# Performance work log

Hardware: AMD Instinct MI355X
Metric: run time of the kernel (lower is better)

## Reference

```python
import jax, jax.numpy as jnp
import numpy as np

N_USERS = 100000
N_ITEMS = 50000
N_EDGES = 2000000
D = 64
EPS = 1e-12  # F.normalize default eps


def setup_inputs() -> dict:
    key = jax.random.key(0)
    k1, k2, k3, k4 = jax.random.split(key, 4)
    x = jax.random.normal(k1, (N_USERS + N_ITEMS, D), dtype=jnp.float32)
    beta = jax.random.normal(k2, (N_USERS,), dtype=jnp.float32) * 0.1
    u = jax.random.randint(k3, (N_EDGES,), 0, N_USERS)
    i = jax.random.randint(k4, (N_EDGES,), 0, N_ITEMS)
    ones = jnp.ones((N_EDGES,), jnp.float32)
    # degree vectors (clamped to >=1 so sqrt-normalization is well-defined)
    du = jnp.maximum(jax.ops.segment_sum(ones, u, num_segments=N_USERS), 1.0)
    di = jnp.maximum(jax.ops.segment_sum(ones, i, num_segments=N_ITEMS), 1.0)
    return {"x": x, "beta": beta, "du": du, "di": di, "u": u, "i": i}


def reference(x, beta, du, di, u, i):
    # split into user/item blocks
    xu, xi = x[:N_USERS], x[N_USERS:]
    # row-wise L2 normalize (torch F.normalize)
    z = x / jnp.maximum(jnp.linalg.norm(x, axis=1, keepdims=True), EPS)
    zu, zi = z[:N_USERS], z[N_USERS:]
    # per-edge score and omega weight: 4/((1+e^-s)(1+e^s)) == 4*sig(s)*(1-sig(s))
    s = jnp.sum(zu[u] * zi[i], axis=1) - beta[u]          # [E]
    sig = jax.nn.sigmoid(s)
    w = 4.0 * sig * (1.0 - sig)
    w = w / jnp.sqrt(du[u]) / jnp.sqrt(di[i])             # degree normalization
    w = w[:, None]                                        # [E,1]
    # scatter-add aggregation back to users and items
    dxu = jax.ops.segment_sum(w * xi[i], u, num_segments=N_USERS)  # [n,D]
    dxi = jax.ops.segment_sum(w * xu[u], i, num_segments=N_ITEMS)  # [m,D]
    return jnp.concatenate([dxu, dxi], axis=0)
```

## Files before the change

kernel.cpp:

```cpp
#include <hip/hip_runtime.h>
#include <math.h>

#define N_USERS 100000
#define N_ITEMS 50000
#define NR      150000
#define N_EDGES 2000000
#define D       64
#define EPS     1e-12f

#define UPAD 64
#define IPAD 80
#define OVF_CAP 4096

#define NPART 8
#define UPP 12500
#define IPP 6250
#define FILL_BPP 256

#define SCAL_OFF 0u
#define XH_OFF   2400000u
#define CNT_OFF  21600000u
#define UBKT_OFF 22200000u
#define IBKT_OFF 35000000u
#define OVFC_OFF 51000000u
#define OVF_OFF  51000004u
#define WS_A3    51016388u

#define C_SCAL 0u
#define C_HEAD 2400000u
#define C_NXTU 3000000u
#define C_NXTI 11000000u
#define WS_C   19000000u

__device__ __forceinline__ unsigned short f2bf(float v) {
    unsigned int b = __float_as_uint(v);
    b += 0x7FFFu + ((b >> 16) & 1u);
    return (unsigned short)(b >> 16);
}
#define BF_LO(w) __uint_as_float((w) << 16)
#define BF_HI(w) __uint_as_float((w) & 0xFFFF0000u)

__global__ void prep_kernel(const float* __restrict__ x,
                            const float* __restrict__ beta,
                            const float* __restrict__ du,
                            const float* __restrict__ di,
                            float4* __restrict__ scal,
                            unsigned short* __restrict__ xh) {
    int gid  = blockIdx.x * blockDim.x + threadIdx.x;
    int r    = gid >> 6;
    int lane = gid & 63;
    if (r >= NR) return;

    float v = x[r * D + lane];
    xh[r * D + lane] = f2bf(v);

    float ss = v * v;
    #pragma unroll
    for (int m = 32; m >= 1; m >>= 1) ss += __shfl_xor(ss, m);

    if (lane == 0) {
        float invn = 1.0f / fmaxf(sqrtf(ss), EPS);
        float deg  = (r < N_USERS) ? du[r] : di[r - N_USERS];
        float b    = (r < N_USERS) ? beta[r] : 0.0f;
        scal[r] = make_float4(invn, rsqrtf(deg), b, 0.0f);
    }
}

__global__ void fillx_kernel(const int* __restrict__ u,
                             const int* __restrict__ i,
                             int* __restrict__ cnt,
                             unsigned short* __restrict__ ubkt,
                             unsigned int* __restrict__ ibkt,
                             int* __restrict__ ovfc,
                             int* __restrict__ ovf) {
    int p   = blockIdx.x & (NPART - 1);
    int q   = blockIdx.x >> 3;
    int tid = q * blockDim.x + threadIdx.x;
    const int stride = FILL_BPP * 256;

    int ulo = p * UPP, uhi = ulo + UPP;
    int ilo = p * IPP, ihi = ilo + IPP;

    for (int e = tid; e < N_EDGES; e += stride) {
        int uu = __builtin_nontemporal_load(u + e);
        int ii = __builtin_nontemporal_load(i + e);

        if (uu >= ulo && uu < uhi) {
            int s = atomicAdd(&cnt[uu], 1);
            if (s < UPAD) {
                ubkt[(size_t)uu * UPAD + s] = (unsigned short)ii;
            } else {
                int pp = atomicAdd(ovfc, 1);
                if (pp < OVF_CAP) ovf[pp] = (e << 1);
            }
        }
        if (ii >= ilo && ii < ihi) {
            int s = atomicAdd(&cnt[N_USERS + ii], 1);
            if (s < IPAD) {
                ibkt[(size_t)ii * IPAD + s] = (unsigned int)uu;
            } else {
                int pp = atomicAdd(ovfc, 1);
                if (pp < OVF_CAP) ovf[pp] = (e << 1) | 1;
            }
        }
    }
}

__global__ void gatherU_kernel(const unsigned short* __restrict__ xh,
                               const float4* __restrict__ scal,
                               const int* __restrict__ cnt,
                               const unsigned short* __restrict__ ubkt,
                               float* __restrict__ out) {
    int gid  = blockIdx.x * blockDim.x + threadIdx.x;
    int r    = gid >> 6;
    int lane = gid & 63;
    if (r >= N_USERS) return;

    int g = lane >> 3;
    int q = lane & 7;

    float4 sc = scal[r];
    uint4 hs = *(const uint4*)(xh + (size_t)r * D + q * 8);
    float xs0 = BF_LO(hs.x), xs1 = BF_HI(hs.x);
    float xs2 = BF_LO(hs.y), xs3 = BF_HI(hs.y);
    float xs4 = BF_LO(hs.z), xs5 = BF_HI(hs.z);
    float xs6 = BF_LO(hs.w), xs7 = BF_HI(hs.w);

    int deg = cnt[r];
    if (deg > UPAD) deg = UPAD;
    int iters = (deg + 7) >> 3;

    float a0=0.f,a1=0.f,a2=0.f,a3=0.f,a4=0.f,a5=0.f,a6=0.f,a7=0.f;

    for (int it = 0; it < iters; ++it) {
        int idx = it * 8 + g;
        bool valid = (idx < deg);
        int nb = N_USERS + (int)ubkt[(size_t)r * UPAD + (valid ? idx : 0)];

        float4 so = scal[nb];
        uint4 ho = *(const uint4*)(xh + (size_t)nb * D + q * 8);
        float o0 = BF_LO(ho.x), o1 = BF_HI(ho.x);
        float o2 = BF_LO(ho.y), o3 = BF_HI(ho.y);
        float o4 = BF_LO(ho.z), o5 = BF_HI(ho.z);
        float o6 = BF_LO(ho.w), o7 = BF_HI(ho.w);

        float p = xs0*o0 + xs1*o1 + xs2*o2 + xs3*o3
                + xs4*o4 + xs5*o5 + xs6*o6 + xs7*o7;
        p += __shfl_xor(p, 1);
        p += __shfl_xor(p, 2);
        p += __shfl_xor(p, 4);

        float sv  = p * sc.x * so.x - sc.z;
        float sig = 1.0f / (1.0f + __expf(-sv));
        float w   = 4.0f * sig * (1.0f - sig) * sc.y * so.y;
        w = valid ? w : 0.0f;

        a0 = fmaf(w, o0, a0); a1 = fmaf(w, o1, a1);
        a2 = fmaf(w, o2, a2); a3 = fmaf(w, o3, a3);
        a4 = fmaf(w, o4, a4); a5 = fmaf(w, o5, a5);
        a6 = fmaf(w, o6, a6); a7 = fmaf(w, o7, a7);
    }

    #pragma unroll
    for (int m = 8; m <= 32; m <<= 1) {
        a0 += __shfl_xor(a0, m); a1 += __shfl_xor(a1, m);
        a2 += __shfl_xor(a2, m); a3 += __shfl_xor(a3, m);
        a4 += __shfl_xor(a4, m); a5 += __shfl_xor(a5, m);
        a6 += __shfl_xor(a6, m); a7 += __shfl_xor(a7, m);
    }

    if (g == 0) {
        float4* o4p = (float4*)(out + (size_t)r * D + q * 8);
        o4p[0] = make_float4(a0, a1, a2, a3);
        o4p[1] = make_float4(a4, a5, a6, a7);
    }
}

__global__ void gatherI_kernel(const unsigned short* __restrict__ xh,
                               const float4* __restrict__ scal,
                               const int* __restrict__ cnt,
                               const unsigned int* __restrict__ ibkt,
                               float* __restrict__ out) {
    int gid  = blockIdx.x * blockDim.x + threadIdx.x;
    int ri   = gid >> 6;
    int lane = gid & 63;
    if (ri >= N_ITEMS) return;
    int r = N_USERS + ri;

    int g = lane >> 3;
    int q = lane & 7;

    float4 sc = scal[r];
    uint4 hs = *(const uint4*)(xh + (size_t)r * D + q * 8);
    float xs0 = BF_LO(hs.x), xs1 = BF_HI(hs.x);
    float xs2 = BF_LO(hs.y), xs3 = BF_HI(hs.y);
    float xs4 = BF_LO(hs.z), xs5 = BF_HI(hs.z);
    float xs6 = BF_LO(hs.w), xs7 = BF_HI(hs.w);

    int deg = cnt[r];
    if (deg > IPAD) deg = IPAD;
    int iters = (deg + 7) >> 3;

    float a0=0.f,a1=0.f,a2=0.f,a3=0.f,a4=0.f,a5=0.f,a6=0.f,a7=0.f;

    for (int it = 0; it < iters; ++it) {
        int idx = it * 8 + g;
        bool valid = (idx < deg);
        int nb = (int)ibkt[(size_t)ri * IPAD + (valid ? idx : 0)];

        float4 so = scal[nb];
        uint4 ho = *(const uint4*)(xh + (size_t)nb * D + q * 8);
        float o0 = BF_LO(ho.x), o1 = BF_HI(ho.x);
        float o2 = BF_LO(ho.y), o3 = BF_HI(ho.y);
        float o4 = BF_LO(ho.z), o5 = BF_HI(ho.z);
        float o6 = BF_LO(ho.w), o7 = BF_HI(ho.w);

        float p = xs0*o0 + xs1*o1 + xs2*o2 + xs3*o3
                + xs4*o4 + xs5*o5 + xs6*o6 + xs7*o7;
        p += __shfl_xor(p, 1);
        p += __shfl_xor(p, 2);
        p += __shfl_xor(p, 4);

        float sv  = p * sc.x * so.x - so.z;
        float sig = 1.0f / (1.0f + __expf(-sv));
        float w   = 4.0f * sig * (1.0f - sig) * sc.y * so.y;
        w = valid ? w : 0.0f;

        a0 = fmaf(w, o0, a0); a1 = fmaf(w, o1, a1);
        a2 = fmaf(w, o2, a2); a3 = fmaf(w, o3, a3);
        a4 = fmaf(w, o4, a4); a5 = fmaf(w, o5, a5);
        a6 = fmaf(w, o6, a6); a7 = fmaf(w, o7, a7);
    }

    #pragma unroll
    for (int m = 8; m <= 32; m <<= 1) {
        a0 += __shfl_xor(a0, m); a1 += __shfl_xor(a1, m);
        a2 += __shfl_xor(a2, m); a3 += __shfl_xor(a3, m);
        a4 += __shfl_xor(a4, m); a5 += __shfl_xor(a5, m);
        a6 += __shfl_xor(a6, m); a7 += __shfl_xor(a7, m);
    }

    if (g == 0) {
        float4* o4p = (float4*)(out + (size_t)r * D + q * 8);
        o4p[0] = make_float4(a0, a1, a2, a3);
        o4p[1] = make_float4(a4, a5, a6, a7);
    }
}

__global__ void ovf_kernel(const float* __restrict__ x,
                           const float4* __restrict__ scal,
                           const int* __restrict__ u,
                           const int* __restrict__ i,
                           const int* __restrict__ ovfc,
                           const int* __restrict__ ovf,
                           float* __restrict__ out) {
    int n = *ovfc;
    if (n > OVF_CAP) n = OVF_CAP;
    int gid  = blockIdx.x * blockDim.x + threadIdx.x;
    int wave = gid >> 6;
    int lane = gid & 63;
    int nw   = (gridDim.x * blockDim.x) >> 6;

    for (int k = wave; k < n; k += nw) {
        int pk = ovf[k];
        int e = pk >> 1, side = pk & 1;
        int uu = u[e];
        int ir = N_USERS + i[e];
        float xu = x[uu * D + lane];
        float xi = x[ir * D + lane];
        float p = xu * xi;
        #pragma unroll
        for (int m = 32; m >= 1; m >>= 1) p += __shfl_xor(p, m);
        float4 su = scal[uu];
        float4 si = scal[ir];
        float sv  = p * su.x * si.x - su.z;
        float sig = 1.0f / (1.0f + __expf(-sv));
        float w   = 4.0f * sig * (1.0f - sig) * su.y * si.y;
        if (side == 0) atomicAdd(&out[(size_t)uu * D + lane], w * xi);
        else           atomicAdd(&out[(size_t)ir * D + lane], w * xu);
    }
}

__global__ void scal_kernel(const float* __restrict__ x,
                            const float* __restrict__ beta,
                            const float* __restrict__ du,
                            const float* __restrict__ di,
                            float4* __restrict__ scal) {
    int gid  = blockIdx.x * blockDim.x + threadIdx.x;
    int r    = gid >> 6;
    int lane = gid & 63;
    if (r >= NR) return;
    float v  = x[r * D + lane];
    float ss = v * v;
    #pragma unroll
    for (int m = 32; m >= 1; m >>= 1) ss += __shfl_xor(ss, m);
    if (lane == 0) {
        float invn = 1.0f / fmaxf(sqrtf(ss), EPS);
        float deg  = (r < N_USERS) ? du[r] : di[r - N_USERS];
        float b    = (r < N_USERS) ? beta[r] : 0.0f;
        scal[r] = make_float4(invn, rsqrtf(deg), b, 0.0f);
    }
}

__global__ void link_kernel(const int* __restrict__ u,
                            const int* __restrict__ i,
                            int* __restrict__ head,
                            int* __restrict__ next_u,
                            int* __restrict__ next_i) {
    int e = blockIdx.x * blockDim.x + threadIdx.x;
    if (e >= N_EDGES) return;
    int uu = u[e];
    int ii = N_USERS + i[e];
    next_u[e] = atomicExch(&head[uu], e);
    next_i[e] = atomicExch(&head[ii], e);
}

__global__ void gather_kernel(const float4* __restrict__ x4,
                              const float4* __restrict__ scal,
                              const int* __restrict__ head,
                              const int* __restrict__ next_u,
                              const int* __restrict__ next_i,
                              const int* __restrict__ u,
                              const int* __restrict__ i,
                              float4* __restrict__ out4) {
    int gid  = blockIdx.x * blockDim.x + threadIdx.x;
    int r    = gid >> 6;
    int lane = gid & 63;
    if (r >= NR) return;
    int g = lane >> 4;
    int q = lane & 15;
    bool isu = (r < N_USERS);
    const int* __restrict__ nxt = isu ? next_u : next_i;
    const int* __restrict__ oid = isu ? i : u;
    int obase = isu ? N_USERS : 0;
    float4 sc = scal[r];
    float4 xs = x4[r * 16 + q];
    float4 acc = make_float4(0.f, 0.f, 0.f, 0.f);
    int e  = head[r];
    int c0 = e; { int t = nxt[(c0 >= 0) ? c0 : 0]; e = (c0 >= 0) ? t : -1; }
    int c1 = e; { int t = nxt[(c1 >= 0) ? c1 : 0]; e = (c1 >= 0) ? t : -1; }
    int c2 = e; { int t = nxt[(c2 >= 0) ? c2 : 0]; e = (c2 >= 0) ? t : -1; }
    int c3 = e; { int t = nxt[(c3 >= 0) ? c3 : 0]; e = (c3 >= 0) ? t : -1; }
    while (c0 >= 0) {
        int n0 = e; { int t = nxt[(n0 >= 0) ? n0 : 0]; e = (n0 >= 0) ? t : -1; }
        int n1 = e; { int t = nxt[(n1 >= 0) ? n1 : 0]; e = (n1 >= 0) ? t : -1; }
        int n2 = e; { int t = nxt[(n2 >= 0) ? n2 : 0]; e = (n2 >= 0) ? t : -1; }
        int n3 = e; { int t = nxt[(n3 >= 0) ? n3 : 0]; e = (n3 >= 0) ? t : -1; }
        int eg = (g == 0) ? c0 : (g == 1) ? c1 : (g == 2) ? c2 : c3;
        bool valid = (eg >= 0);
        int  es = valid ? eg : c0;
        int  nb = obase + oid[es];
        float4 so = scal[nb];
        float4 xo = x4[nb * 16 + q];
        float p = xs.x * xo.x + xs.y * xo.y + xs.z * xo.z + xs.w * xo.w;
        p += __shfl_xor(p, 1);
        p += __shfl_xor(p, 2);
        p += __shfl_xor(p, 4);
        p += __shfl_xor(p, 8);
        float b   = isu ? sc.z : so.z;
        float sv  = p * sc.x * so.x - b;
        float sig = 1.0f / (1.0f + __expf(-sv));
        float w   = 4.0f * sig * (1.0f - sig) * sc.y * so.y;
        w = valid ? w : 0.0f;
        acc.x = fmaf(w, xo.x, acc.x);
        acc.y = fmaf(w, xo.y, acc.y);
        acc.z = fmaf(w, xo.z, acc.z);
        acc.w = fmaf(w, xo.w, acc.w);
        c0 = n0; c1 = n1; c2 = n2; c3 = n3;
    }
    acc.x += __shfl_xor(acc.x, 16); acc.y += __shfl_xor(acc.y, 16);
    acc.z += __shfl_xor(acc.z, 16); acc.w += __shfl_xor(acc.w, 16);
    acc.x += __shfl_xor(acc.x, 32); acc.y += __shfl_xor(acc.y, 32);
    acc.z += __shfl_xor(acc.z, 32); acc.w += __shfl_xor(acc.w, 32);
    if (g == 0) out4[r * 16 + q] = acc;
}

__global__ void norm_kernel(const float* __restrict__ x,
                            float* __restrict__ invn,
                            int nrows) {
    int gid  = blockIdx.x * blockDim.x + threadIdx.x;
    int wave = gid >> 6;
    int lane = gid & 63;
    if (wave >= nrows) return;
    float v  = x[wave * D + lane];
    float ss = v * v;
    #pragma unroll
    for (int m = 32; m >= 1; m >>= 1) ss += __shfl_xor(ss, m);
    if (lane == 0) invn[wave] = 1.0f / fmaxf(sqrtf(ss), EPS);
}

__global__ void edge_kernel(const float* __restrict__ x,
                            const float* __restrict__ beta,
                            const float* __restrict__ du,
                            const float* __restrict__ di,
                            const int*   __restrict__ u,
                            const int*   __restrict__ i,
                            const float* __restrict__ invn,
                            float* __restrict__ out) {
    int gid  = blockIdx.x * blockDim.x + threadIdx.x;
    int wave = gid >> 6;
    int lane = gid & 63;
    if (wave >= N_EDGES) return;
    int uu = u[wave];
    int ii = i[wave];
    const float xu = x[uu * D + lane];
    const float xi = x[(N_USERS + ii) * D + lane];
    float p = xu * xi;
    #pragma unroll
    for (int m = 32; m >= 1; m >>= 1) p += __shfl_xor(p, m);
    float s   = p * invn[uu] * invn[N_USERS + ii] - beta[uu];
    float sig = 1.0f / (1.0f + __expf(-s));
    float w   = 4.0f * sig * (1.0f - sig) * rsqrtf(du[uu]) * rsqrtf(di[ii]);
    atomicAdd(&out[uu * D + lane],             w * xi);
    atomicAdd(&out[(N_USERS + ii) * D + lane], w * xu);
}

extern "C" void kernel_launch(void* const* d_in, const int* in_sizes, int n_in,
                              void* d_out, int out_size, void* d_ws, size_t ws_size,
                              hipStream_t stream) {
    const float* x    = (const float*)d_in[0];
    const float* beta = (const float*)d_in[1];
    const float* du   = (const float*)d_in[2];
    const float* di   = (const float*)d_in[3];
    const int*   u    = (const int*)d_in[4];
    const int*   i    = (const int*)d_in[5];
    float* out = (float*)d_out;
    char*  ws  = (char*)d_ws;

    if (ws_size >= (size_t)WS_A3) {
        float4*         scal = (float4*)(ws + SCAL_OFF);
        unsigned short* xh   = (unsigned short*)(ws + XH_OFF);
        int*            cnt  = (int*)(ws + CNT_OFF);
        unsigned short* ubkt = (unsigned short*)(ws + UBKT_OFF);
        unsigned int*   ibkt = (unsigned int*)(ws + IBKT_OFF);
        int*            ovfc = (int*)(ws + OVFC_OFF);
        int*            ovf  = (int*)(ws + OVF_OFF);

        prep_kernel<<<(NR + 3) / 4, 256, 0, stream>>>(x, beta, du, di, scal, xh);
        hipMemsetAsync(cnt, 0, (size_t)NR * sizeof(int), stream);
        hipMemsetAsync(ovfc, 0, sizeof(int), stream);
        fillx_kernel<<<NPART * FILL_BPP, 256, 0, stream>>>(u, i, cnt, ubkt, ibkt, ovfc, ovf);
        gatherU_kernel<<<(N_USERS + 3) / 4, 256, 0, stream>>>(xh, scal, cnt, ubkt, out);
        gatherI_kernel<<<(N_ITEMS + 3) / 4, 256, 0, stream>>>(xh, scal, cnt, ibkt, out);
        ovf_kernel<<<64, 256, 0, stream>>>(x, scal, u, i, ovfc, ovf, out);
    } else if (ws_size >= (size_t)WS_C) {
        float4* scal   = (float4*)(ws + C_SCAL);
        int*    head   = (int*)(ws + C_HEAD);
        int*    next_u = (int*)(ws + C_NXTU);
        int*    next_i = (int*)(ws + C_NXTI);

        scal_kernel<<<(NR + 3) / 4, 256, 0, stream>>>(x, beta, du, di, scal);
        hipMemsetAsync(head, 0xFF, (size_t)NR * sizeof(int), stream);
        link_kernel<<<(N_EDGES + 255) / 256, 256, 0, stream>>>(u, i, head, next_u, next_i);
        gather_kernel<<<(NR + 3) / 4, 256, 0, stream>>>((const float4*)x, scal, head,
                                                        next_u, next_i, u, i, (float4*)out);
    } else {
        float* invn = (float*)ws;
        hipMemsetAsync(d_out, 0, (size_t)out_size * sizeof(float), stream);
        norm_kernel<<<(NR + 3) / 4, 256, 0, stream>>>(x, invn, NR);
        edge_kernel<<<(N_EDGES + 3) / 4, 256, 0, stream>>>(x, beta, du, di, u, i, invn, out);
    }
}
```

Before: 317.6 us.

## Fuse prep into fill kernel, merge user/item gathers, halve fill partitions

Merges the prep pass into the bucket-fill kernel as extra blocks, so row normalization and bf16 conversion run alongside the edge bucketing. The separate user and item gather kernels become one launch. Each fill block now scans the edge list twice over two smaller node sub-ranges, aiming at better cache locality for the atomics and bucket writes at the cost of reading the edge arrays twice. The item bucket pad drops from 80 to 64, shrinking the workspace but sending more edges to the overflow atomic path, which is capped at 4096 entries.

```diff
diff --git a/kernel.cpp b/kernel.cpp
--- a/kernel.cpp
+++ b/kernel.cpp
@@ -9,22 +9,26 @@
 #define EPS     1e-12f
 
 #define UPAD 64
-#define IPAD 80
+#define IPAD 64
 #define OVF_CAP 4096
 
 #define NPART 8
-#define UPP 12500
-#define IPP 6250
+#define NSUB  2
+#define NCHUNK (NPART * NSUB)
+#define UCH (N_USERS / NCHUNK)
+#define ICH (N_ITEMS / NCHUNK)
 #define FILL_BPP 256
+#define FILL_BLOCKS (NPART * FILL_BPP)
+#define PREP_BLOCKS ((NR + 3) / 4)
 
 #define SCAL_OFF 0u
 #define XH_OFF   2400000u
 #define CNT_OFF  21600000u
 #define UBKT_OFF 22200000u
 #define IBKT_OFF 35000000u
-#define OVFC_OFF 51000000u
-#define OVF_OFF  51000004u
-#define WS_A3    51016388u
+#define OVFC_OFF 47800000u
+#define OVF_OFF  47800004u
+#define WS_A4    47816388u
 
 #define C_SCAL 0u
 #define C_HEAD 2400000u
@@ -40,81 +44,88 @@
 #define BF_LO(w) __uint_as_float((w) << 16)
 #define BF_HI(w) __uint_as_float((w) & 0xFFFF0000u)
 
-__global__ void prep_kernel(const float* __restrict__ x,
-                            const float* __restrict__ beta,
-                            const float* __restrict__ du,
-                            const float* __restrict__ di,
-                            float4* __restrict__ scal,
-                            unsigned short* __restrict__ xh) {
-    int gid  = blockIdx.x * blockDim.x + threadIdx.x;
-    int r    = gid >> 6;
-    int lane = gid & 63;
-    if (r >= NR) return;
-
-    float v = x[r * D + lane];
-    xh[r * D + lane] = f2bf(v);
-
-    float ss = v * v;
-    #pragma unroll
-    for (int m = 32; m >= 1; m >>= 1) ss += __shfl_xor(ss, m);
-
-    if (lane == 0) {
-        float invn = 1.0f / fmaxf(sqrtf(ss), EPS);
-        float deg  = (r < N_USERS) ? du[r] : di[r - N_USERS];
-        float b    = (r < N_USERS) ? beta[r] : 0.0f;
-        scal[r] = make_float4(invn, rsqrtf(deg), b, 0.0f);
-    }
-}
-
-__global__ void fillx_kernel(const int* __restrict__ u,
-                             const int* __restrict__ i,
-                             int* __restrict__ cnt,
-                             unsigned short* __restrict__ ubkt,
-                             unsigned int* __restrict__ ibkt,
-                             int* __restrict__ ovfc,
-                             int* __restrict__ ovf) {
-    int p   = blockIdx.x & (NPART - 1);
-    int q   = blockIdx.x >> 3;
-    int tid = q * blockDim.x + threadIdx.x;
-    const int stride = FILL_BPP * 256;
-
-    int ulo = p * UPP, uhi = ulo + UPP;
-    int ilo = p * IPP, ihi = ilo + IPP;
-
-    for (int e = tid; e < N_EDGES; e += stride) {
-        int uu = __builtin_nontemporal_load(u + e);
-        int ii = __builtin_nontemporal_load(i + e);
-
-        if (uu >= ulo && uu < uhi) {
-            int s = atomicAdd(&cnt[uu], 1);
-            if (s < UPAD) {
-                ubkt[(size_t)uu * UPAD + s] = (unsigned short)ii;
-            } else {
-                int pp = atomicAdd(ovfc, 1);
-                if (pp < OVF_CAP) ovf[pp] = (e << 1);
+__global__ void fillprep_kernel(const float* __restrict__ x,
+                                const float* __restrict__ beta,
+                                const float* __restrict__ du,
+                                const float* __restrict__ di,
+                                float4* __restrict__ scal,
+                                unsigned short* __restrict__ xh,
+                                const int* __restrict__ u,
+                                const int* __restrict__ i,
+                                int* __restrict__ cnt,
+                                unsigned short* __restrict__ ubkt,
+                                unsigned int* __restrict__ ibkt,
+                                int* __restrict__ ovfc,
+                                int* __restrict__ ovf) {
+    if (blockIdx.x < FILL_BLOCKS) {
+        int p   = blockIdx.x & (NPART - 1);
+        int qb  = blockIdx.x >> 3;
+        int tid = qb * blockDim.x + threadIdx.x;
+        const int stride = FILL_BPP * 256;
+
+        #pragma unroll
+        for (int sub = 0; sub < NSUB; ++sub) {
+            int c   = p * NSUB + sub;
+            int ulo = c * UCH, uhi = ulo + UCH;
+            int ilo = c * ICH, ihi = ilo + ICH;
+
+            for (int e = tid; e < N_EDGES; e += stride) {
+                int uu = __builtin_nontemporal_load(u + e);
+                int ii = __builtin_nontemporal_load(i + e);
+
+                if (uu >= ulo && uu < uhi) {
+                    int s = atomicAdd(&cnt[uu], 1);
+                    if (s < UPAD) {
+                        ubkt[(size_t)uu * UPAD + s] = (unsigned short)ii;
+                    } else {
+                        int pp = atomicAdd(ovfc, 1);
+                        if (pp < OVF_CAP) ovf[pp] = (e << 1);
+                    }
+                }
+                if (ii >= ilo && ii < ihi) {
+                    int s = atomicAdd(&cnt[N_USERS + ii], 1);
+                    if (s < IPAD) {
+                        ibkt[(size_t)ii * IPAD + s] = (unsigned int)uu;
+                    } else {
+                        int pp = atomicAdd(ovfc, 1);
+                        if (pp < OVF_CAP) ovf[pp] = (e << 1) | 1;
+                    }
+                }
             }
         }
-        if (ii >= ilo && ii < ihi) {
-            int s = atomicAdd(&cnt[N_USERS + ii], 1);
-            if (s < IPAD) {
-                ibkt[(size_t)ii * IPAD + s] = (unsigned int)uu;
-            } else {
-                int pp = atomicAdd(ovfc, 1);
-                if (pp < OVF_CAP) ovf[pp] = (e << 1) | 1;
-            }
+    } else {
+        int b    = blockIdx.x - FILL_BLOCKS;
+        int gid  = b * blockDim.x + threadIdx.x;
+        int r    = gid >> 6;
+        int lane = gid & 63;
+        if (r >= NR) return;
+
+        float v = x[r * D + lane];
+        xh[r * D + lane] = f2bf(v);
+
+        float ss = v * v;
+        #pragma unroll
+        for (int m = 32; m >= 1; m >>= 1) ss += __shfl_xor(ss, m);
+
+        if (lane == 0) {
+            float invn = 1.0f / fmaxf(sqrtf(ss), EPS);
+            float deg  = (r < N_USERS) ? du[r] : di[r - N_USERS];
+            float bb   = (r < N_USERS) ? beta[r] : 0.0f;
+            scal[r] = make_float4(invn, rsqrtf(deg), bb, 0.0f);
         }
     }
 }
 
-__global__ void gatherU_kernel(const unsigned short* __restrict__ xh,
+__global__ void gatherA_kernel(const unsigned short* __restrict__ xh,
                                const float4* __restrict__ scal,
                                const int* __restrict__ cnt,
                                const unsigned short* __restrict__ ubkt,
+                               const unsigned int* __restrict__ ibkt,
                                float* __restrict__ out) {
     int gid  = blockIdx.x * blockDim.x + threadIdx.x;
     int r    = gid >> 6;
     int lane = gid & 63;
-    if (r >= N_USERS) return;
+    if (r >= NR) return;
 
     int g = lane >> 3;
     int q = lane & 7;
@@ -126,110 +137,75 @@
     float xs4 = BF_LO(hs.z), xs5 = BF_HI(hs.z);
     float xs6 = BF_LO(hs.w), xs7 = BF_HI(hs.w);
 
-    int deg = cnt[r];
-    if (deg > UPAD) deg = UPAD;
-    int iters = (deg + 7) >> 3;
-
     float a0=0.f,a1=0.f,a2=0.f,a3=0.f,a4=0.f,a5=0.f,a6=0.f,a7=0.f;
 
-    for (int it = 0; it < iters; ++it) {
-        int idx = it * 8 + g;
-        bool valid = (idx < deg);
-        int nb = N_USERS + (int)ubkt[(size_t)r * UPAD + (valid ? idx : 0)];
-
-        float4 so = scal[nb];
-        uint4 ho = *(const uint4*)(xh + (size_t)nb * D + q * 8);
-        float o0 = BF_LO(ho.x), o1 = BF_HI(ho.x);
-        float o2 = BF_LO(ho.y), o3 = BF_HI(ho.y);
-        float o4 = BF_LO(ho.z), o5 = BF_HI(ho.z);
-        float o6 = BF_LO(ho.w), o7 = BF_HI(ho.w);
-
-        float p = xs0*o0 + xs1*o1 + xs2*o2 + xs3*o3
-                + xs4*o4 + xs5*o5 + xs6*o6 + xs7*o7;
-        p += __shfl_xor(p, 1);
-        p += __shfl_xor(p, 2);
-        p += __shfl_xor(p, 4);
-
-        float sv  = p * sc.x * so.x - sc.z;
-        float sig = 1.0f / (1.0f + __expf(-sv));
-        float w   = 4.0f * sig * (1.0f - sig) * sc.y * so.y;
-        w = valid ? w : 0.0f;
-
-        a0 = fmaf(w, o0, a0); a1 = fmaf(w, o1, a1);
-        a2 = fmaf(w, o2, a2); a3 = fmaf(w, o3, a3);
-        a4 = fmaf(w, o4, a4); a5 = fmaf(w, o5, a5);
-        a6 = fmaf(w, o6, a6); a7 = fmaf(w, o7, a7);
-    }
-
-    #pragma unroll
-    for (int m = 8; m <= 32; m <<= 1) {
-        a0 += __shfl_xor(a0, m); a1 += __shfl_xor(a1, m);
-        a2 += __shfl_xor(a2, m); a3 += __shfl_xor(a3, m);
-        a4 += __shfl_xor(a4, m); a5 += __shfl_xor(a5, m);
-        a6 += __shfl_xor(a6, m); a7 += __shfl_xor(a7, m);
-    }
-
-    if (g == 0) {
-        float4* o4p = (float4*)(out + (size_t)r * D + q * 8);
-        o4p[0] = make_float4(a0, a1, a2, a3);
-        o4p[1] = make_float4(a4, a5, a6, a7);
-    }
-}
-
-__global__ void gatherI_kernel(const unsigned short* __restrict__ xh,
-                               const float4* __restrict__ scal,
-                               const int* __restrict__ cnt,
-                               const unsigned int* __restrict__ ibkt,
-                               float* __restrict__ out) {
-    int gid  = blockIdx.x * blockDim.x + threadIdx.x;
-    int ri   = gid >> 6;
-    int lane = gid & 63;
-    if (ri >= N_ITEMS) return;
-    int r = N_USERS + ri;
-
-    int g = lane >> 3;
-    int q = lane & 7;
-
-    float4 sc = scal[r];
-    uint4 hs = *(const uint4*)(xh + (size_t)r * D + q * 8);
-    float xs0 = BF_LO(hs.x), xs1 = BF_HI(hs.x);
-    float xs2 = BF_LO(hs.y), xs3 = BF_HI(hs.y);
-    float xs4 = BF_LO(hs.z), xs5 = BF_HI(hs.z);
-    float xs6 = BF_LO(hs.w), xs7 = BF_HI(hs.w);
-
-    int deg = cnt[r];
-    if (deg > IPAD) deg = IPAD;
-    int iters = (deg + 7) >> 3;
-
-    float a0=0.f,a1=0.f,a2=0.f,a3=0.f,a4=0.f,a5=0.f,a6=0.f,a7=0.f;
-
-    for (int it = 0; it < iters; ++it) {
-        int idx = it * 8 + g;
-        bool valid = (idx < deg);
-        int nb = (int)ibkt[(size_t)ri * IPAD + (valid ? idx : 0)];
-
-        float4 so = scal[nb];
-        uint4 ho = *(const uint4*)(xh + (size_t)nb * D + q * 8);
-        float o0 = BF_LO(ho.x), o1 = BF_HI(ho.x);
-        float o2 = BF_LO(ho.y), o3 = BF_HI(ho.y);
-        float o4 = BF_LO(ho.z), o5 = BF_HI(ho.z);
-        float o6 = BF_LO(ho.w), o7 = BF_HI(ho.w);
-
-        float p = xs0*o0 + xs1*o1 + xs2*o2 + xs3*o3
-                + xs4*o4 + xs5*o5 + xs6*o6 + xs7*o7;
-        p += __shfl_xor(p, 1);
-        p += __shfl_xor(p, 2);
-        p += __shfl_xor(p, 4);
-
-        float sv  = p * sc.x * so.x - so.z;
-        float sig = 1.0f / (1.0f + __expf(-sv));
-        float w   = 4.0f * sig * (1.0f - sig) * sc.y * so.y;
-        w = valid ? w : 0.0f;
-
-        a0 = fmaf(w, o0, a0); a1 = fmaf(w, o1, a1);
-        a2 = fmaf(w, o2, a2); a3 = fmaf(w, o3, a3);
-        a4 = fmaf(w, o4, a4); a5 = fmaf(w, o5, a5);
-        a6 = fmaf(w, o6, a6); a7 = fmaf(w, o7, a7);
+    if (r < N_USERS) {
+        int deg = cnt[r];
+        if (deg > UPAD) deg = UPAD;
+        int iters = (deg + 7) >> 3;
+
+        for (int it = 0; it < iters; ++it) {
+            int idx = it * 8 + g;
+            bool valid = (idx < deg);
+            int nb = N_USERS + (int)ubkt[(size_t)r * UPAD + (valid ? idx : 0)];
+
+            float4 so = scal[nb];
+            uint4 ho = *(const uint4*)(xh + (size_t)nb * D + q * 8);
+            float o0 = BF_LO(ho.x), o1 = BF_HI(ho.x);
+            float o2 = BF_LO(ho.y), o3 = BF_HI(ho.y);
+            float o4 = BF_LO(ho.z), o5 = BF_HI(ho.z);
+            float o6 = BF_LO(ho.w), o7 = BF_HI(ho.w);
+
+            float p = xs0*o0 + xs1*o1 + xs2*o2 + xs3*o3
+                    + xs4*o4 + xs5*o5 + xs6*o6 + xs7*o7;
+            p += __shfl_xor(p, 1);
+            p += __shfl_xor(p, 2);
+            p += __shfl_xor(p, 4);
+
+            float sv  = p * sc.x * so.x - sc.z;
+            float sig = 1.0f / (1.0f + __expf(-sv));
+            float w   = 4.0f * sig * (1.0f - sig) * sc.y * so.y;
+            w = valid ? w : 0.0f;
+
+            a0 = fmaf(w, o0, a0); a1 = fmaf(w, o1, a1);
+            a2 = fmaf(w, o2, a2); a3 = fmaf(w, o3, a3);
+            a4 = fmaf(w, o4, a4); a5 = fmaf(w, o5, a5);
+            a6 = fmaf(w, o6, a6); a7 = fmaf(w, o7, a7);
+        }
+    } else {
+        int ri = r - N_USERS;
+        int deg = cnt[r];
+        if (deg > IPAD) deg = IPAD;
+        int iters = (deg + 7) >> 3;
+
+        for (int it = 0; it < iters; ++it) {
+            int idx = it * 8 + g;
+            bool valid = (idx < deg);
+            int nb = (int)ibkt[(size_t)ri * IPAD + (valid ? idx : 0)];
+
+            float4 so = scal[nb];
+            uint4 ho = *(const uint4*)(xh + (size_t)nb * D + q * 8);
+            float o0 = BF_LO(ho.x), o1 = BF_HI(ho.x);
+            float o2 = BF_LO(ho.y), o3 = BF_HI(ho.y);
+            float o4 = BF_LO(ho.z), o5 = BF_HI(ho.z);
+            float o6 = BF_LO(ho.w), o7 = BF_HI(ho.w);
+
+            float p = xs0*o0 + xs1*o1 + xs2*o2 + xs3*o3
+                    + xs4*o4 + xs5*o5 + xs6*o6 + xs7*o7;
+            p += __shfl_xor(p, 1);
+            p += __shfl_xor(p, 2);
+            p += __shfl_xor(p, 4);
+
+            float sv  = p * sc.x * so.x - so.z;
+            float sig = 1.0f / (1.0f + __expf(-sv));
+            float w   = 4.0f * sig * (1.0f - sig) * sc.y * so.y;
+            w = valid ? w : 0.0f;
+
+            a0 = fmaf(w, o0, a0); a1 = fmaf(w, o1, a1);
+            a2 = fmaf(w, o2, a2); a3 = fmaf(w, o3, a3);
+            a4 = fmaf(w, o4, a4); a5 = fmaf(w, o5, a5);
+            a6 = fmaf(w, o6, a6); a7 = fmaf(w, o7, a7);
+        }
     }
 
     #pragma unroll
@@ -427,7 +403,7 @@
     float* out = (float*)d_out;
     char*  ws  = (char*)d_ws;
 
-    if (ws_size >= (size_t)WS_A3) {
+    if (ws_size >= (size_t)WS_A4) {
         float4*         scal = (float4*)(ws + SCAL_OFF);
         unsigned short* xh   = (unsigned short*)(ws + XH_OFF);
         int*            cnt  = (int*)(ws + CNT_OFF);
@@ -436,12 +412,11 @@
         int*            ovfc = (int*)(ws + OVFC_OFF);
         int*            ovf  = (int*)(ws + OVF_OFF);
 
-        prep_kernel<<<(NR + 3) / 4, 256, 0, stream>>>(x, beta, du, di, scal, xh);
         hipMemsetAsync(cnt, 0, (size_t)NR * sizeof(int), stream);
         hipMemsetAsync(ovfc, 0, sizeof(int), stream);
-        fillx_kernel<<<NPART * FILL_BPP, 256, 0, stream>>>(u, i, cnt, ubkt, ibkt, ovfc, ovf);
-        gatherU_kernel<<<(N_USERS + 3) / 4, 256, 0, stream>>>(xh, scal, cnt, ubkt, out);
-        gatherI_kernel<<<(N_ITEMS + 3) / 4, 256, 0, stream>>>(xh, scal, cnt, ibkt, out);
+        fillprep_kernel<<<FILL_BLOCKS + PREP_BLOCKS, 256, 0, stream>>>(
+            x, beta, du, di, scal, xh, u, i, cnt, ubkt, ibkt, ovfc, ovf);
+        gatherA_kernel<<<(NR + 3) / 4, 256, 0, stream>>>(xh, scal, cnt, ubkt, ibkt, out);
         ovf_kernel<<<64, 256, 0, stream>>>(x, scal, u, i, ovfc, ovf, out);
     } else if (ws_size >= (size_t)WS_C) {
         float4* scal   = (float4*)(ws + C_SCAL);
```

After: 350.6 us. 10.4% more time.

## Pre-normalize bf16 embeddings, fold degree scaling, and shrink bucket padding

Applied to the files above, without the earlier changes.

The prep kernel now stores L2-normalized bf16 rows. It also packs rsqrt(deg)*norm into the spare scal slot, so the gather loops drop two scalar multiplies per edge and apply the row's own degree factor once at output. User and item bucket padding is reduced (64→48, 80→64), and overflow records store explicit (dest, neighbor) pairs, so the overflow kernel no longer re-reads u/i. The linked-list fallback path is deleted. The risks are more overflow edges handled by slow atomics, and a slight precision change from normalizing before the bf16 rounding.

```diff
diff --git a/kernel.cpp b/kernel.cpp
--- a/kernel.cpp
+++ b/kernel.cpp
@@ -8,29 +8,23 @@
 #define D       64
 #define EPS     1e-12f
 
-#define UPAD 64
-#define IPAD 80
+#define UPAD 48
+#define IPAD 64
 #define OVF_CAP 4096
 
 #define NPART 8
-#define UPP 12500
-#define IPP 6250
-#define FILL_BPP 256
+#define UCH (N_USERS / NPART)
+#define ICH (N_ITEMS / NPART)
+#define FILL_BLOCKS 2048
 
 #define SCAL_OFF 0u
 #define XH_OFF   2400000u
 #define CNT_OFF  21600000u
 #define UBKT_OFF 22200000u
-#define IBKT_OFF 35000000u
-#define OVFC_OFF 51000000u
-#define OVF_OFF  51000004u
-#define WS_A3    51016388u
-
-#define C_SCAL 0u
-#define C_HEAD 2400000u
-#define C_NXTU 3000000u
-#define C_NXTI 11000000u
-#define WS_C   19000000u
+#define IBKT_OFF 31800000u
+#define OVFC_OFF 44600000u
+#define OVF_OFF  44600008u
+#define WS_MAIN  44632776u
 
 __device__ __forceinline__ unsigned short f2bf(float v) {
     unsigned int b = __float_as_uint(v);
@@ -51,18 +45,20 @@
     int lane = gid & 63;
     if (r >= NR) return;
 
-    float v = x[r * D + lane];
-    xh[r * D + lane] = f2bf(v);
-
+    float v  = x[r * D + lane];
     float ss = v * v;
     #pragma unroll
     for (int m = 32; m >= 1; m >>= 1) ss += __shfl_xor(ss, m);
 
+    float nrm  = fmaxf(sqrtf(ss), EPS);
+    float invn = 1.0f / nrm;
+    xh[r * D + lane] = f2bf(v * invn);
+
     if (lane == 0) {
-        float invn = 1.0f / fmaxf(sqrtf(ss), EPS);
-        float deg  = (r < N_USERS) ? du[r] : di[r - N_USERS];
-        float b    = (r < N_USERS) ? beta[r] : 0.0f;
-        scal[r] = make_float4(invn, rsqrtf(deg), b, 0.0f);
+        float deg = (r < N_USERS) ? du[r] : di[r - N_USERS];
+        float bb  = (r < N_USERS) ? beta[r] : 0.0f;
+        float rsd = rsqrtf(deg);
+        scal[r] = make_float4(invn, rsd, bb, rsd * nrm);
     }
 }
 
@@ -72,14 +68,14 @@
                              unsigned short* __restrict__ ubkt,
                              unsigned int* __restrict__ ibkt,
                              int* __restrict__ ovfc,
-                             int* __restrict__ ovf) {
+                             int2* __restrict__ ovf) {
     int p   = blockIdx.x & (NPART - 1);
-    int q   = blockIdx.x >> 3;
-    int tid = q * blockDim.x + threadIdx.x;
-    const int stride = FILL_BPP * 256;
-
-    int ulo = p * UPP, uhi = ulo + UPP;
-    int ilo = p * IPP, ihi = ilo + IPP;
+    int qb  = blockIdx.x >> 3;
+    int tid = qb * blockDim.x + threadIdx.x;
+    const int stride = (FILL_BLOCKS / NPART) * 256;
+
+    int ulo = p * UCH, uhi = ulo + UCH;
+    int ilo = p * ICH, ihi = ilo + ICH;
 
     for (int e = tid; e < N_EDGES; e += stride) {
         int uu = __builtin_nontemporal_load(u + e);
@@ -91,7 +87,7 @@
                 ubkt[(size_t)uu * UPAD + s] = (unsigned short)ii;
             } else {
                 int pp = atomicAdd(ovfc, 1);
-                if (pp < OVF_CAP) ovf[pp] = (e << 1);
+                if (pp < OVF_CAP) ovf[pp] = make_int2(uu, N_USERS + ii);
             }
         }
         if (ii >= ilo && ii < ihi) {
@@ -100,7 +96,7 @@
                 ibkt[(size_t)ii * IPAD + s] = (unsigned int)uu;
             } else {
                 int pp = atomicAdd(ovfc, 1);
-                if (pp < OVF_CAP) ovf[pp] = (e << 1) | 1;
+                if (pp < OVF_CAP) ovf[pp] = make_int2(N_USERS + ii, uu);
             }
         }
     }
@@ -144,21 +140,21 @@
         float o4 = BF_LO(ho.z), o5 = BF_HI(ho.z);
         float o6 = BF_LO(ho.w), o7 = BF_HI(ho.w);
 
-        float p = xs0*o0 + xs1*o1 + xs2*o2 + xs3*o3
-                + xs4*o4 + xs5*o5 + xs6*o6 + xs7*o7;
-        p += __shfl_xor(p, 1);
-        p += __shfl_xor(p, 2);
-        p += __shfl_xor(p, 4);
-
-        float sv  = p * sc.x * so.x - sc.z;
+        float pd = xs0*o0 + xs1*o1 + xs2*o2 + xs3*o3
+                 + xs4*o4 + xs5*o5 + xs6*o6 + xs7*o7;
+        pd += __shfl_xor(pd, 1);
+        pd += __shfl_xor(pd, 2);
+        pd += __shfl_xor(pd, 4);
+
+        float sv  = pd - sc.z;
         float sig = 1.0f / (1.0f + __expf(-sv));
-        float w   = 4.0f * sig * (1.0f - sig) * sc.y * so.y;
-        w = valid ? w : 0.0f;
-
-        a0 = fmaf(w, o0, a0); a1 = fmaf(w, o1, a1);
-        a2 = fmaf(w, o2, a2); a3 = fmaf(w, o3, a3);
-        a4 = fmaf(w, o4, a4); a5 = fmaf(w, o5, a5);
-        a6 = fmaf(w, o6, a6); a7 = fmaf(w, o7, a7);
+        float t4  = 4.0f * sig * (1.0f - sig) * so.w;
+        t4 = valid ? t4 : 0.0f;
+
+        a0 = fmaf(t4, o0, a0); a1 = fmaf(t4, o1, a1);
+        a2 = fmaf(t4, o2, a2); a3 = fmaf(t4, o3, a3);
+        a4 = fmaf(t4, o4, a4); a5 = fmaf(t4, o5, a5);
+        a6 = fmaf(t4, o6, a6); a7 = fmaf(t4, o7, a7);
     }
 
     #pragma unroll
@@ -170,9 +166,10 @@
     }
 
     if (g == 0) {
+        float rsd = sc.y;
         float4* o4p = (float4*)(out + (size_t)r * D + q * 8);
-        o4p[0] = make_float4(a0, a1, a2, a3);
-        o4p[1] = make_float4(a4, a5, a6, a7);
+        o4p[0] = make_float4(a0*rsd, a1*rsd, a2*rsd, a3*rsd);
+        o4p[1] = make_float4(a4*rsd, a5*rsd, a6*rsd, a7*rsd);
     }
 }
 
@@ -215,21 +212,21 @@
         float o4 = BF_LO(ho.z), o5 = BF_HI(ho.z);
         float o6 = BF_LO(ho.w), o7 = BF_HI(ho.w);
 
-        float p = xs0*o0 + xs1*o1 + xs2*o2 + xs3*o3
-                + xs4*o4 + xs5*o5 + xs6*o6 + xs7*o7;
-        p += __shfl_xor(p, 1);
-        p += __shfl_xor(p, 2);
-        p += __shfl_xor(p, 4);
-
-        float sv  = p * sc.x * so.x - so.z;
+        float pd = xs0*o0 + xs1*o1 + xs2*o2 + xs3*o3
+                 + xs4*o4 + xs5*o5 + xs6*o6 + xs7*o7;
+        pd += __shfl_xor(pd, 1);
+        pd += __shfl_xor(pd, 2);
+        pd += __shfl_xor(pd, 4);
+
+        float sv  = pd - so.z;
         float sig = 1.0f / (1.0f + __expf(-sv));
-        float w   = 4.0f * sig * (1.0f - sig) * sc.y * so.y;
-        w = valid ? w : 0.0f;
-
-        a0 = fmaf(w, o0, a0); a1 = fmaf(w, o1, a1);
-        a2 = fmaf(w, o2, a2); a3 = fmaf(w, o3, a3);
-        a4 = fmaf(w, o4, a4); a5 = fmaf(w, o5, a5);
-        a6 = fmaf(w, o6, a6); a7 = fmaf(w, o7, a7);
+        float t4  = 4.0f * sig * (1.0f - sig) * so.w;
+        t4 = valid ? t4 : 0.0f;
+
+        a0 = fmaf(t4, o0, a0); a1 = fmaf(t4, o1, a1);
+        a2 = fmaf(t4, o2, a2); a3 = fmaf(t4, o3, a3);
+        a4 = fmaf(t4, o4, a4); a5 = fmaf(t4, o5, a5);
+        a6 = fmaf(t4, o6, a6); a7 = fmaf(t4, o7, a7);
     }
 
     #pragma unroll
@@ -241,146 +238,45 @@
     }
 
     if (g == 0) {
+        float rsd = sc.y;
         float4* o4p = (float4*)(out + (size_t)r * D + q * 8);
-        o4p[0] = make_float4(a0, a1, a2, a3);
-        o4p[1] = make_float4(a4, a5, a6, a7);
-    }
-}
-
-__global__ void ovf_kernel(const float* __restrict__ x,
-                           const float4* __restrict__ scal,
-                           const int* __restrict__ u,
-                           const int* __restrict__ i,
-                           const int* __restrict__ ovfc,
-                           const int* __restrict__ ovf,
-                           float* __restrict__ out) {
+        o4p[0] = make_float4(a0*rsd, a1*rsd, a2*rsd, a3*rsd);
+        o4p[1] = make_float4(a4*rsd, a5*rsd, a6*rsd, a7*rsd);
+    }
+}
+
+__global__ void ovf2_kernel(const float* __restrict__ x,
+                            const float4* __restrict__ scal,
+                            const int* __restrict__ ovfc,
+                            const int2* __restrict__ ovf,
+                            float* __restrict__ out) {
     int n = *ovfc;
     if (n > OVF_CAP) n = OVF_CAP;
     int gid  = blockIdx.x * blockDim.x + threadIdx.x;
-    int wave = gid >> 6;
-    int lane = gid & 63;
+    int wave = gid >> 6, lane = gid & 63;
     int nw   = (gridDim.x * blockDim.x) >> 6;
 
     for (int k = wave; k < n; k += nw) {
-        int pk = ovf[k];
-        int e = pk >> 1, side = pk & 1;
-        int uu = u[e];
-        int ir = N_USERS + i[e];
-        float xu = x[uu * D + lane];
-        float xi = x[ir * D + lane];
-        float p = xu * xi;
+        int d  = ovf[k].x;
+        int nb = ovf[k].y;
+        float xd = x[(size_t)d * D + lane];
+        float xn = x[(size_t)nb * D + lane];
+        float pd = xd * xn;
         #pragma unroll
-        for (int m = 32; m >= 1; m >>= 1) p += __shfl_xor(p, m);
-        float4 su = scal[uu];
-        float4 si = scal[ir];
-        float sv  = p * su.x * si.x - su.z;
+        for (int m = 32; m >= 1; m >>= 1) pd += __shfl_xor(pd, m);
+        float4 sd = scal[d];
+        float4 sn = scal[nb];
+        float sv  = pd * sd.x * sn.x - (sd.z + sn.z);
         float sig = 1.0f / (1.0f + __expf(-sv));
-        float w   = 4.0f * sig * (1.0f - sig) * su.y * si.y;
-        if (side == 0) atomicAdd(&out[(size_t)uu * D + lane], w * xi);
-        else           atomicAdd(&out[(size_t)ir * D + lane], w * xu);
-    }
-}
-
-__global__ void scal_kernel(const float* __restrict__ x,
-                            const float* __restrict__ beta,
-                            const float* __restrict__ du,
-                            const float* __restrict__ di,
-                            float4* __restrict__ scal) {
-    int gid  = blockIdx.x * blockDim.x + threadIdx.x;
-    int r    = gid >> 6;
-    int lane = gid & 63;
-    if (r >= NR) return;
-    float v  = x[r * D + lane];
-    float ss = v * v;
-    #pragma unroll
-    for (int m = 32; m >= 1; m >>= 1) ss += __shfl_xor(ss, m);
-    if (lane == 0) {
-        float invn = 1.0f / fmaxf(sqrtf(ss), EPS);
-        float deg  = (r < N_USERS) ? du[r] : di[r - N_USERS];
-        float b    = (r < N_USERS) ? beta[r] : 0.0f;
-        scal[r] = make_float4(invn, rsqrtf(deg), b, 0.0f);
-    }
-}
-
-__global__ void link_kernel(const int* __restrict__ u,
-                            const int* __restrict__ i,
-                            int* __restrict__ head,
-                            int* __restrict__ next_u,
-                            int* __restrict__ next_i) {
-    int e = blockIdx.x * blockDim.x + threadIdx.x;
-    if (e >= N_EDGES) return;
-    int uu = u[e];
-    int ii = N_USERS + i[e];
-    next_u[e] = atomicExch(&head[uu], e);
-    next_i[e] = atomicExch(&head[ii], e);
-}
-
-__global__ void gather_kernel(const float4* __restrict__ x4,
-                              const float4* __restrict__ scal,
-                              const int* __restrict__ head,
-                              const int* __restrict__ next_u,
-                              const int* __restrict__ next_i,
-                              const int* __restrict__ u,
-                              const int* __restrict__ i,
-                              float4* __restrict__ out4) {
-    int gid  = blockIdx.x * blockDim.x + threadIdx.x;
-    int r    = gid >> 6;
-    int lane = gid & 63;
-    if (r >= NR) return;
-    int g = lane >> 4;
-    int q = lane & 15;
-    bool isu = (r < N_USERS);
-    const int* __restrict__ nxt = isu ? next_u : next_i;
-    const int* __restrict__ oid = isu ? i : u;
-    int obase = isu ? N_USERS : 0;
-    float4 sc = scal[r];
-    float4 xs = x4[r * 16 + q];
-    float4 acc = make_float4(0.f, 0.f, 0.f, 0.f);
-    int e  = head[r];
-    int c0 = e; { int t = nxt[(c0 >= 0) ? c0 : 0]; e = (c0 >= 0) ? t : -1; }
-    int c1 = e; { int t = nxt[(c1 >= 0) ? c1 : 0]; e = (c1 >= 0) ? t : -1; }
-    int c2 = e; { int t = nxt[(c2 >= 0) ? c2 : 0]; e = (c2 >= 0) ? t : -1; }
-    int c3 = e; { int t = nxt[(c3 >= 0) ? c3 : 0]; e = (c3 >= 0) ? t : -1; }
-    while (c0 >= 0) {
-        int n0 = e; { int t = nxt[(n0 >= 0) ? n0 : 0]; e = (n0 >= 0) ? t : -1; }
-        int n1 = e; { int t = nxt[(n1 >= 0) ? n1 : 0]; e = (n1 >= 0) ? t : -1; }
-        int n2 = e; { int t = nxt[(n2 >= 0) ? n2 : 0]; e = (n2 >= 0) ? t : -1; }
-        int n3 = e; { int t = nxt[(n3 >= 0) ? n3 : 0]; e = (n3 >= 0) ? t : -1; }
-        int eg = (g == 0) ? c0 : (g == 1) ? c1 : (g == 2) ? c2 : c3;
-        bool valid = (eg >= 0);
-        int  es = valid ? eg : c0;
-        int  nb = obase + oid[es];
-        float4 so = scal[nb];
-        float4 xo = x4[nb * 16 + q];
-        float p = xs.x * xo.x + xs.y * xo.y + xs.z * xo.z + xs.w * xo.w;
-        p += __shfl_xor(p, 1);
-        p += __shfl_xor(p, 2);
-        p += __shfl_xor(p, 4);
-        p += __shfl_xor(p, 8);
-        float b   = isu ? sc.z : so.z;
-        float sv  = p * sc.x * so.x - b;
-        float sig = 1.0f / (1.0f + __expf(-sv));
-        float w   = 4.0f * sig * (1.0f - sig) * sc.y * so.y;
-        w = valid ? w : 0.0f;
-        acc.x = fmaf(w, xo.x, acc.x);
-        acc.y = fmaf(w, xo.y, acc.y);
-        acc.z = fmaf(w, xo.z, acc.z);
-        acc.w = fmaf(w, xo.w, acc.w);
-        c0 = n0; c1 = n1; c2 = n2; c3 = n3;
-    }
-    acc.x += __shfl_xor(acc.x, 16); acc.y += __shfl_xor(acc.y, 16);
-    acc.z += __shfl_xor(acc.z, 16); acc.w += __shfl_xor(acc.w, 16);
-    acc.x += __shfl_xor(acc.x, 32); acc.y += __shfl_xor(acc.y, 32);
-    acc.z += __shfl_xor(acc.z, 32); acc.w += __shfl_xor(acc.w, 32);
-    if (g == 0) out4[r * 16 + q] = acc;
+        float w   = 4.0f * sig * (1.0f - sig) * sd.y * sn.y;
+        atomicAdd(&out[(size_t)d * D + lane], w * xn);
+    }
 }
 
 __global__ void norm_kernel(const float* __restrict__ x,
-                            float* __restrict__ invn,
-                            int nrows) {
-    int gid  = blockIdx.x * blockDim.x + threadIdx.x;
-    int wave = gid >> 6;
-    int lane = gid & 63;
+                            float* __restrict__ invn, int nrows) {
+    int gid  = blockIdx.x * blockDim.x + threadIdx.x;
+    int wave = gid >> 6, lane = gid & 63;
     if (wave >= nrows) return;
     float v  = x[wave * D + lane];
     float ss = v * v;
@@ -393,18 +289,16 @@
                             const float* __restrict__ beta,
                             const float* __restrict__ du,
                             const float* __restrict__ di,
-                            const int*   __restrict__ u,
-                            const int*   __restrict__ i,
+                            const int* __restrict__ u,
+                            const int* __restrict__ i,
                             const float* __restrict__ invn,
                             float* __restrict__ out) {
     int gid  = blockIdx.x * blockDim.x + threadIdx.x;
-    int wave = gid >> 6;
-    int lane = gid & 63;
+    int wave = gid >> 6, lane = gid & 63;
     if (wave >= N_EDGES) return;
-    int uu = u[wave];
-    int ii = i[wave];
-    const float xu = x[uu * D + lane];
-    const float xi = x[(N_USERS + ii) * D + lane];
+    int uu = u[wave], ii = i[wave];
+    float xu = x[uu * D + lane];
+    float xi = x[(N_USERS + ii) * D + lane];
     float p = xu * xi;
     #pragma unroll
     for (int m = 32; m >= 1; m >>= 1) p += __shfl_xor(p, m);
@@ -427,33 +321,22 @@
     float* out = (float*)d_out;
     char*  ws  = (char*)d_ws;
 
-    if (ws_size >= (size_t)WS_A3) {
+    if (ws_size >= (size_t)WS_MAIN) {
         float4*         scal = (float4*)(ws + SCAL_OFF);
         unsigned short* xh   = (unsigned short*)(ws + XH_OFF);
         int*            cnt  = (int*)(ws + CNT_OFF);
         unsigned short* ubkt = (unsigned short*)(ws + UBKT_OFF);
         unsigned int*   ibkt = (unsigned int*)(ws + IBKT_OFF);
         int*            ovfc = (int*)(ws + OVFC_OFF);
-        int*            ovf  = (int*)(ws + OVF_OFF);
-
-        prep_kernel<<<(NR + 3) / 4, 256, 0, stream>>>(x, beta, du, di, scal, xh);
+        int2*           ovf  = (int2*)(ws + OVF_OFF);
+
         hipMemsetAsync(cnt, 0, (size_t)NR * sizeof(int), stream);
         hipMemsetAsync(ovfc, 0, sizeof(int), stream);
-        fillx_kernel<<<NPART * FILL_BPP, 256, 0, stream>>>(u, i, cnt, ubkt, ibkt, ovfc, ovf);
+        prep_kernel<<<(NR + 3) / 4, 256, 0, stream>>>(x, beta, du, di, scal, xh);
+        fillx_kernel<<<FILL_BLOCKS, 256, 0, stream>>>(u, i, cnt, ubkt, ibkt, ovfc, ovf);
         gatherU_kernel<<<(N_USERS + 3) / 4, 256, 0, stream>>>(xh, scal, cnt, ubkt, out);
         gatherI_kernel<<<(N_ITEMS + 3) / 4, 256, 0, stream>>>(xh, scal, cnt, ibkt, out);
-        ovf_kernel<<<64, 256, 0, stream>>>(x, scal, u, i, ovfc, ovf, out);
-    } else if (ws_size >= (size_t)WS_C) {
-        float4* scal   = (float4*)(ws + C_SCAL);
-        int*    head   = (int*)(ws + C_HEAD);
-        int*    next_u = (int*)(ws + C_NXTU);
-        int*    next_i = (int*)(ws + C_NXTI);
-
-        scal_kernel<<<(NR + 3) / 4, 256, 0, stream>>>(x, beta, du, di, scal);
-        hipMemsetAsync(head, 0xFF, (size_t)NR * sizeof(int), stream);
-        link_kernel<<<(N_EDGES + 255) / 256, 256, 0, stream>>>(u, i, head, next_u, next_i);
-        gather_kernel<<<(NR + 3) / 4, 256, 0, stream>>>((const float4*)x, scal, head,
-                                                        next_u, next_i, u, i, (float4*)out);
+        ovf2_kernel<<<64, 256, 0, stream>>>(x, scal, ovfc, ovf, out);
     } else {
         float* invn = (float*)ws;
         hipMemsetAsync(d_out, 0, (size_t)out_size * sizeof(float), stream);
```

Measured after the change: 322.2 us. No clear change (+1.5%).
